# Kernel tuning notes

Measured on AMD Instinct MI355X. Metric: run time of the kernel, lower is better.

The kernel has to match this reference:

```python
import math
import jax, jax.numpy as jnp
import numpy as np

FS = 96000.0
N_BIQUADS = 16
HPF_FREQ_RANGE = (20.0, 500.0)
LPF_FREQ_RANGE = (5000.0, 20000.0)
SHELF_FREQ_RANGE = (50.0, 16000.0)
PEAK_FREQ_RANGE = (100.0, 15000.0)
Q_RANGE = (0.5, 16.0)
GAIN_RANGE = (-24.0, 24.0)
BROADBAND_RANGE = (-60.0, 0.0)


def _denorm_log(norm, lo, hi):
    return jnp.exp(math.log(lo) + norm * (math.log(hi) - math.log(lo)))


def _coef_highpass(fc, Q):
    w0 = 2.0 * math.pi * fc / FS
    alpha = jnp.sin(w0) / (2.0 * Q)
    c = jnp.cos(w0)
    b0 = (1 + c) / 2; b1 = -(1 + c); b2 = (1 + c) / 2
    a0 = 1 + alpha; a1 = -2 * c; a2 = 1 - alpha
    return b0 / a0, b1 / a0, b2 / a0, a1 / a0, a2 / a0


def _coef_lowpass(fc, Q):
    w0 = 2.0 * math.pi * fc / FS
    alpha = jnp.sin(w0) / (2.0 * Q)
    c = jnp.cos(w0)
    b0 = (1 - c) / 2; b1 = 1 - c; b2 = (1 - c) / 2
    a0 = 1 + alpha; a1 = -2 * c; a2 = 1 - alpha
    return b0 / a0, b1 / a0, b2 / a0, a1 / a0, a2 / a0


def _coef_lowshelf(fc, gain_db, Q):
    A = 10.0 ** (gain_db / 40.0)
    w0 = 2.0 * math.pi * fc / FS
    alpha = jnp.sin(w0) / (2.0 * Q)
    c = jnp.cos(w0)
    sA = jnp.sqrt(A)
    b0 = A * (A + 1 - (A - 1) * c + 2 * sA * alpha)
    b1 = 2 * A * (A - 1 - (A + 1) * c)
    b2 = A * (A + 1 - (A - 1) * c - 2 * sA * alpha)
    a0 = A + 1 + (A - 1) * c + 2 * sA * alpha
    a1 = -2 * (A - 1 + (A + 1) * c)
    a2 = A + 1 + (A - 1) * c - 2 * sA * alpha
    return b0 / a0, b1 / a0, b2 / a0, a1 / a0, a2 / a0


def _coef_highshelf(fc, gain_db, Q):
    A = 10.0 ** (gain_db / 40.0)
    w0 = 2.0 * math.pi * fc / FS
    alpha = jnp.sin(w0) / (2.0 * Q)
    c = jnp.cos(w0)
    sA = jnp.sqrt(A)
    b0 = A * (A + 1 + (A - 1) * c + 2 * sA * alpha)
    b1 = -2 * A * (A - 1 + (A + 1) * c)
    b2 = A * (A + 1 + (A - 1) * c - 2 * sA * alpha)
    a0 = A + 1 - (A - 1) * c + 2 * sA * alpha
    a1 = 2 * (A - 1 - (A + 1) * c)
    a2 = A + 1 - (A - 1) * c - 2 * sA * alpha
    return b0 / a0, b1 / a0, b2 / a0, a1 / a0, a2 / a0


def _coef_peak(fc, gain_db, Q):
    A = 10.0 ** (gain_db / 40.0)
    w0 = 2.0 * math.pi * fc / FS
    alpha = jnp.sin(w0) / (2.0 * Q)
    c = jnp.cos(w0)
    b0 = 1 + alpha * A; b1 = -2 * c; b2 = 1 - alpha * A
    a0 = 1 + alpha / A; a1 = -2 * c; a2 = 1 - alpha / A
    return b0 / a0, b1 / a0, b2 / a0, a1 / a0, a2 / a0


def _biquad(x, coefs):
    # x: (B, T); coefs: 5 arrays of shape (B,)
    b0, b1, b2, a1, a2 = coefs

    def step(carry, xt):  # xt: (B,)
        s1, s2 = carry
        y = b0 * xt + s1
        return (b1 * xt - a1 * y + s2, b2 * xt - a2 * y), y

    z = jnp.zeros(x.shape[0], x.dtype)
    _, ys = jax.lax.scan(step, (z, z), x.T)  # ys: (T, B)
    return ys.T


def _chain(audio, params):
    B = audio.shape[0]
    bp = params[:, :N_BIQUADS * 3].reshape(B, N_BIQUADS, 3)
    bb_lo, bb_hi = BROADBAND_RANGE
    in_db = bb_lo + params[:, -2] * (bb_hi - bb_lo)
    out_db = bb_lo + params[:, -1] * (bb_hi - bb_lo)
    x = audio * (10.0 ** (in_db / 20.0))[:, None]

    for i in range(N_BIQUADS):
        fn, gn, qn = bp[:, i, 0], bp[:, i, 1], bp[:, i, 2]
        Q = _denorm_log(qn, *Q_RANGE)
        gain = GAIN_RANGE[0] + gn * (GAIN_RANGE[1] - GAIN_RANGE[0])
        if i == 0:  # HPF
            coefs = _coef_highpass(_denorm_log(fn, *HPF_FREQ_RANGE), Q)
        elif i == 15:  # LPF
            coefs = _coef_lowpass(_denorm_log(fn, *LPF_FREQ_RANGE), Q)
        elif i == 1:  # low shelf
            coefs = _coef_lowshelf(_denorm_log(fn, *SHELF_FREQ_RANGE), gain, Q)
        elif i == 14:  # high shelf
            coefs = _coef_highshelf(_denorm_log(fn, *SHELF_FREQ_RANGE), gain, Q)
        else:  # peaking EQ
            coefs = _coef_peak(_denorm_log(fn, *PEAK_FREQ_RANGE), gain, Q)
        x = _biquad(x, coefs)

    return x * (10.0 ** (out_db / 20.0))[:, None]


def setup_inputs() -> dict:
    key = jax.random.key(0)
    k1, k2 = jax.random.split(key)
    audio = jax.random.normal(k1, (16, 262144), dtype=jnp.float32)
    params = jax.random.uniform(k2, (16, 50), dtype=jnp.float32)
    return {"audio": audio, "params": params}


def reference(audio, params):
    return _chain(audio, params)
```

## Files before the change

### kernel.cpp

```cpp
#include <hip/hip_runtime.h>
#include <math.h>

#define BATCH   16
#define T_LEN   262144
#define NB      16
#define L       64
#define GRP     64
#define SUB     16
#define CHAINS  4
#define NSUB    256
#define NSUP    16
#define NG      64
#define NCHUNK  4096
#define XSTRIDE 68

#define DPI 3.14159265358979323846264338327950288

#define OFF_COEF  0
#define OFF_A64   1536
#define OFF_A1K   17920
#define OFF_A16K  34304
#define OFF_QEND  50688
#define OFF_SARR  181760
#define OFF_P     312832

__device__ inline void stage_coefs(int i, double fn, double gn, double qn,
                                   double& B0, double& B1, double& B2,
                                   double& A1, double& A2) {
    const double FS = 96000.0;
    double Q    = exp(log(0.5) + qn * (log(16.0) - log(0.5)));
    double gain = -24.0 + gn * 48.0;
    double lo, hi;
    if (i == 0)            { lo = 20.0;   hi = 500.0;   }
    else if (i == 15)      { lo = 5000.0; hi = 20000.0; }
    else if (i == 1 || i == 14) { lo = 50.0; hi = 16000.0; }
    else                   { lo = 100.0;  hi = 15000.0; }
    double fc    = exp(log(lo) + fn * (log(hi) - log(lo)));
    double w0    = 2.0 * DPI * fc / FS;
    double alpha = sin(w0) / (2.0 * Q);
    double c     = cos(w0);
    double b0, b1, b2, a0, a1, a2;
    if (i == 0) {
        b0 = (1.0 + c) * 0.5; b1 = -(1.0 + c); b2 = (1.0 + c) * 0.5;
        a0 = 1.0 + alpha; a1 = -2.0 * c; a2 = 1.0 - alpha;
    } else if (i == 15) {
        b0 = (1.0 - c) * 0.5; b1 = 1.0 - c; b2 = (1.0 - c) * 0.5;
        a0 = 1.0 + alpha; a1 = -2.0 * c; a2 = 1.0 - alpha;
    } else if (i == 1) {
        double A = pow(10.0, gain / 40.0), sA = sqrt(A);
        b0 = A * ((A + 1.0) - (A - 1.0) * c + 2.0 * sA * alpha);
        b1 = 2.0 * A * ((A - 1.0) - (A + 1.0) * c);
        b2 = A * ((A + 1.0) - (A - 1.0) * c - 2.0 * sA * alpha);
        a0 = (A + 1.0) + (A - 1.0) * c + 2.0 * sA * alpha;
        a1 = -2.0 * ((A - 1.0) + (A + 1.0) * c);
        a2 = (A + 1.0) + (A - 1.0) * c - 2.0 * sA * alpha;
    } else if (i == 14) {
        double A = pow(10.0, gain / 40.0), sA = sqrt(A);
        b0 = A * ((A + 1.0) + (A - 1.0) * c + 2.0 * sA * alpha);
        b1 = -2.0 * A * ((A - 1.0) + (A + 1.0) * c);
        b2 = A * ((A + 1.0) + (A - 1.0) * c - 2.0 * sA * alpha);
        a0 = (A + 1.0) - (A - 1.0) * c + 2.0 * sA * alpha;
        a1 = 2.0 * ((A - 1.0) - (A + 1.0) * c);
        a2 = (A + 1.0) - (A - 1.0) * c - 2.0 * sA * alpha;
    } else {
        double A = pow(10.0, gain / 40.0);
        b0 = 1.0 + alpha * A; b1 = -2.0 * c; b2 = 1.0 - alpha * A;
        a0 = 1.0 + alpha / A; a1 = -2.0 * c; a2 = 1.0 - alpha / A;
    }
    B0 = b0 / a0; B1 = b1 / a0; B2 = b2 / a0; A1 = a1 / a0; A2 = a2 / a0;
}

__global__ __launch_bounds__(256) void k0_setup(const float* __restrict__ params,
                                                float* __restrict__ coefs,
                                                float* __restrict__ A64,
                                                float* __restrict__ A1K,
                                                float* __restrict__ A16K) {
    int b = blockIdx.x;
    int t = threadIdx.x;
    __shared__ double cf[NB][5];
    __shared__ double M1[32 * 32];
    __shared__ double M2[32 * 32];

    if (t < NB) {
        double B0, B1, B2, A1, A2;
        stage_coefs(t, (double)params[b * 50 + t * 3 + 0],
                       (double)params[b * 50 + t * 3 + 1],
                       (double)params[b * 50 + t * 3 + 2], B0, B1, B2, A1, A2);
        float f0 = (float)B0, f1 = (float)B1, f2 = (float)B2, f3 = (float)A1, f4 = (float)A2;
        cf[t][0] = (double)f0; cf[t][1] = (double)f1; cf[t][2] = (double)f2;
        cf[t][3] = (double)f3; cf[t][4] = (double)f4;
        float* cp = coefs + b * 96 + t * 5;
        cp[0] = f0; cp[1] = f1; cp[2] = f2; cp[3] = f3; cp[4] = f4;
    }
    if (t == NB) {
        double indb = -60.0 + (double)params[b * 50 + 48] * 60.0;
        coefs[b * 96 + 80] = (float)pow(10.0, indb / 20.0);
    }
    if (t == NB + 1) {
        double outdb = -60.0 + (double)params[b * 50 + 49] * 60.0;
        coefs[b * 96 + 81] = (float)pow(10.0, outdb / 20.0);
    }
    __syncthreads();

    if (t < 32) {
        double s1[NB], s2[NB];
#pragma unroll
        for (int i = 0; i < NB; i++) {
            s1[i] = (t == 2 * i) ? 1.0 : 0.0;
            s2[i] = (t == 2 * i + 1) ? 1.0 : 0.0;
        }
        double u = 0.0;
#pragma unroll
        for (int i = 0; i < NB; i++) {
            double y  = cf[i][0] * u + s1[i];
            double n1 = cf[i][1] * u - cf[i][3] * y + s2[i];
            double n2 = cf[i][2] * u - cf[i][4] * y;
            s1[i] = n1; s2[i] = n2; u = y;
        }
#pragma unroll
        for (int i = 0; i < NB; i++) {
            M1[(2 * i) * 32 + t]     = s1[i];
            M1[(2 * i + 1) * 32 + t] = s2[i];
        }
    }
    __syncthreads();

    int c  = t & 31;
    int r0 = t >> 5;
    double* src = M1;
    double* dst = M2;
    for (int sq = 0; sq < 14; sq++) {
        double acc[4] = {0.0, 0.0, 0.0, 0.0};
        for (int k = 0; k < 32; k++) {
            double bv = src[k * 32 + c];
#pragma unroll
            for (int e = 0; e < 4; e++)
                acc[e] += src[(e * 8 + r0) * 32 + k] * bv;
        }
#pragma unroll
        for (int e = 0; e < 4; e++) dst[(e * 8 + r0) * 32 + c] = acc[e];
        __syncthreads();
        { double* tmp = src; src = dst; dst = tmp; }
        float* out_m = (sq == 5) ? A64 : (sq == 9) ? A1K : (sq == 13) ? A16K : nullptr;
        if (out_m) {
#pragma unroll
            for (int e = 0; e < 4; e++) {
                int idx = (e * 8 + r0) * 32 + c;
                out_m[b * 1024 + idx] = (float)src[idx];
            }
        }
        __syncthreads();
    }
}

__device__ __forceinline__ float mv_step_rl(const float* ar, float q, float addv) {
    int qi = __float_as_int(q);
    float qb[32];
#pragma unroll
    for (int t = 0; t < 32; t++)
        qb[t] = __int_as_float(__builtin_amdgcn_readlane(qi, t));
    float acc0 = addv, acc1 = 0.f;
#pragma unroll
    for (int t = 0; t < 32; t += 2) {
        acc0 = fmaf(ar[t], qb[t], acc0);
        acc1 = fmaf(ar[t + 1], qb[t + 1], acc1);
    }
    return acc0 + acc1;
}

__device__ __forceinline__ void load_row32(const float* base, int row, float* ar) {
    const float4* a4 = (const float4*)(base + row * 32);
#pragma unroll
    for (int j = 0; j < 8; j++) {
        float4 v = a4[j];
        ar[4 * j + 0] = v.x; ar[4 * j + 1] = v.y;
        ar[4 * j + 2] = v.z; ar[4 * j + 3] = v.w;
    }
}

__device__ __forceinline__ void stage_audio(const float* __restrict__ gbase,
                                            float* __restrict__ xlds, int lane) {
    const float4* g4 = (const float4*)gbase;
    float4 v[16];
#pragma unroll
    for (int it = 0; it < 16; it++) v[it] = g4[it * 64 + lane];
#pragma unroll
    for (int it = 0; it < 16; it++) {
        int idx = it * 64 + lane;
        int ch = idx >> 4, q = idx & 15;
        *(float4*)&xlds[ch * XSTRIDE + q * 4] = v[it];
    }
}

__global__ __launch_bounds__(64, 1) void k1_pass1(const float* __restrict__ audio,
                                                  const float* __restrict__ coefs,
                                                  const float* __restrict__ A64,
                                                  float* __restrict__ P,
                                                  float* __restrict__ Qend) {
    int blk   = blockIdx.x;
    int batch = blk >> 6;
    int grp   = blk & 63;
    int lane  = threadIdx.x;
    int row   = lane & 31;

    __shared__ float xlds[GRP * XSTRIDE];
    __shared__ float plds[GRP][33];

    stage_audio(audio + (size_t)batch * T_LEN + (size_t)grp * GRP * L, xlds, lane);
    __syncthreads();

    const float* cf = coefs + batch * 96;
    float c0[NB], c1[NB], c2[NB], c3[NB], c4[NB];
#pragma unroll
    for (int i = 0; i < NB; i++) {
        c0[i] = cf[i * 5 + 0]; c1[i] = cf[i * 5 + 1]; c2[i] = cf[i * 5 + 2];
        c3[i] = cf[i * 5 + 3]; c4[i] = cf[i * 5 + 4];
    }
    float ing = cf[80];

    float s1[NB], s2[NB];
#pragma unroll
    for (int i = 0; i < NB; i++) { s1[i] = 0.f; s2[i] = 0.f; }

    float* xrow = &xlds[lane * XSTRIDE];
#pragma unroll 1
    for (int tt = 0; tt < 16; tt++) {
        float4 xv = *(const float4*)&xrow[tt * 4];
        float xs[4] = {xv.x, xv.y, xv.z, xv.w};
#pragma unroll
        for (int j = 0; j < 4; j++) {
            float u = ing * xs[j];
#pragma unroll
            for (int i = 0; i < NB; i++) {
                float y  = fmaf(c0[i], u, s1[i]);
                float n1 = fmaf(c1[i], u, s2[i]); n1 = fmaf(-c3[i], y, n1);
                float n2 = c2[i] * u;             n2 = fmaf(-c4[i], y, n2);
                s1[i] = n1; s2[i] = n2; u = y;
            }
        }
    }

    {
        float* pb = P + ((size_t)(batch * NG + grp)) * 2048;
#pragma unroll
        for (int i = 0; i < NB; i++) {
            pb[(2 * i) * 64 + lane]     = s1[i];
            pb[(2 * i + 1) * 64 + lane] = s2[i];
        }
    }

#pragma unroll
    for (int i = 0; i < NB; i++) {
        plds[lane][2 * i]     = s1[i];
        plds[lane][2 * i + 1] = s2[i];
    }
    __syncthreads();

    float ar[32];
    load_row32(A64 + batch * 1024, row, ar);
    float q0 = 0.f, q1 = 0.f, q2 = 0.f, q3 = 0.f;
#pragma unroll 1
    for (int j = 0; j < SUB; j++) {
        float p0 = plds[0 * SUB + j][row];
        float p1 = plds[1 * SUB + j][row];
        float p2 = plds[2 * SUB + j][row];
        float p3 = plds[3 * SUB + j][row];
        q0 = mv_step_rl(ar, q0, p0);
        q1 = mv_step_rl(ar, q1, p1);
        q2 = mv_step_rl(ar, q2, p2);
        q3 = mv_step_rl(ar, q3, p3);
    }
    if (lane < 32) {
        float* qe = Qend + ((size_t)(batch * NSUB + grp * CHAINS)) * 32 + row;
        qe[0] = q0; qe[32] = q1; qe[64] = q2; qe[96] = q3;
    }
}

__global__ __launch_bounds__(256, 1) void k2_combine(const float* __restrict__ A1K,
                                                     const float* __restrict__ A16K,
                                                     const float* __restrict__ Qend,
                                                     float* __restrict__ Sarr) {
    int batch = blockIdx.x;
    int tid   = threadIdx.x;
    int wave  = tid >> 6;
    int lane  = tid & 63;
    int row   = lane & 31;

    __shared__ float qe[NSUB][32];
    __shared__ float qs[NSUP][32];
    __shared__ float ss[NSUP][32];

    {
        const float4* src4 = (const float4*)(Qend + (size_t)batch * NSUB * 32);
        float4* dst4 = (float4*)&qe[0][0];
        for (int i = tid; i < NSUB * 32 / 4; i += 256) dst4[i] = src4[i];
    }
    float ar1k[32];
    load_row32(A1K + batch * 1024, row, ar1k);
    __syncthreads();

    int s0i = wave * 4;
    {
        float q0 = 0.f, q1 = 0.f, q2 = 0.f, q3 = 0.f;
#pragma unroll 1
        for (int j = 0; j < 16; j++) {
            float p0 = qe[(s0i + 0) * 16 + j][row];
            float p1 = qe[(s0i + 1) * 16 + j][row];
            float p2 = qe[(s0i + 2) * 16 + j][row];
            float p3 = qe[(s0i + 3) * 16 + j][row];
            q0 = mv_step_rl(ar1k, q0, p0);
            q1 = mv_step_rl(ar1k, q1, p1);
            q2 = mv_step_rl(ar1k, q2, p2);
            q3 = mv_step_rl(ar1k, q3, p3);
        }
        if (lane < 32) {
            qs[s0i + 0][row] = q0; qs[s0i + 1][row] = q1;
            qs[s0i + 2][row] = q2; qs[s0i + 3][row] = q3;
        }
    }
    __syncthreads();

    if (wave == 0) {
        float ark[32];
        load_row32(A16K + batch * 1024, row, ark);
        float S = 0.f;
#pragma unroll 1
        for (int s = 0; s < NSUP; s++) {
            if (lane < 32) ss[s][row] = S;
            float addv = qs[s][row];
            S = mv_step_rl(ark, S, addv);
        }
    }
    __syncthreads();

    {
        float q0 = ss[s0i + 0][row];
        float q1 = ss[s0i + 1][row];
        float q2 = ss[s0i + 2][row];
        float q3 = ss[s0i + 3][row];
#pragma unroll 1
        for (int j = 0; j < 16; j++) {
            if (lane < 32) {
                Sarr[((size_t)(batch * NSUB + (s0i + 0) * 16 + j)) * 32 + row] = q0;
                Sarr[((size_t)(batch * NSUB + (s0i + 1) * 16 + j)) * 32 + row] = q1;
                Sarr[((size_t)(batch * NSUB + (s0i + 2) * 16 + j)) * 32 + row] = q2;
                Sarr[((size_t)(batch * NSUB + (s0i + 3) * 16 + j)) * 32 + row] = q3;
            }
            float p0 = qe[(s0i + 0) * 16 + j][row];
            float p1 = qe[(s0i + 1) * 16 + j][row];
            float p2 = qe[(s0i + 2) * 16 + j][row];
            float p3 = qe[(s0i + 3) * 16 + j][row];
            q0 = mv_step_rl(ar1k, q0, p0);
            q1 = mv_step_rl(ar1k, q1, p1);
            q2 = mv_step_rl(ar1k, q2, p2);
            q3 = mv_step_rl(ar1k, q3, p3);
        }
    }
}

__global__ __launch_bounds__(64, 1) void k3_pass2(const float* __restrict__ audio,
                                                  const float* __restrict__ coefs,
                                                  const float* __restrict__ A64,
                                                  const float* __restrict__ P,
                                                  const float* __restrict__ Sarr,
                                                  float* __restrict__ out) {
    int blk   = blockIdx.x;
    int batch = blk >> 6;
    int grp   = blk & 63;
    int lane  = threadIdx.x;
    int row   = lane & 31;

    __shared__ float xlds[GRP * XSTRIDE];
    __shared__ float plds[GRP][33];

    stage_audio(audio + (size_t)batch * T_LEN + (size_t)grp * GRP * L, xlds, lane);

    {
        const float* pb = P + ((size_t)(batch * NG + grp)) * 2048;
        float pv[32];
#pragma unroll
        for (int s = 0; s < 32; s++) pv[s] = pb[s * 64 + lane];
#pragma unroll
        for (int s = 0; s < 32; s++) plds[lane][s] = pv[s];
    }
    __syncthreads();

    {
        float ar[32];
        load_row32(A64 + batch * 1024, row, ar);
        const float* sp = Sarr + ((size_t)(batch * NSUB + grp * CHAINS)) * 32 + row;
        float q0 = sp[0], q1 = sp[32], q2 = sp[64], q3 = sp[96];
#pragma unroll 1
        for (int j = 0; j < SUB; j++) {
            float p0 = plds[0 * SUB + j][row];
            float p1 = plds[1 * SUB + j][row];
            float p2 = plds[2 * SUB + j][row];
            float p3 = plds[3 * SUB + j][row];
            if (lane < 32) {
                plds[0 * SUB + j][row] = q0;
                plds[1 * SUB + j][row] = q1;
                plds[2 * SUB + j][row] = q2;
                plds[3 * SUB + j][row] = q3;
            }
            q0 = mv_step_rl(ar, q0, p0);
            q1 = mv_step_rl(ar, q1, p1);
            q2 = mv_step_rl(ar, q2, p2);
            q3 = mv_step_rl(ar, q3, p3);
        }
    }
    __syncthreads();

    const float* cf = coefs + batch * 96;
    float c0[NB], c1[NB], c2[NB], c3[NB], c4[NB];
#pragma unroll
    for (int i = 0; i < NB; i++) {
        c0[i] = cf[i * 5 + 0]; c1[i] = cf[i * 5 + 1]; c2[i] = cf[i * 5 + 2];
        c3[i] = cf[i * 5 + 3]; c4[i] = cf[i * 5 + 4];
    }
    float ing  = cf[80];
    float outg = cf[81];

    float s1[NB], s2[NB];
#pragma unroll
    for (int i = 0; i < NB; i++) {
        s1[i] = plds[lane][2 * i];
        s2[i] = plds[lane][2 * i + 1];
    }

    float* xrow = &xlds[lane * XSTRIDE];
#pragma unroll 1
    for (int tt = 0; tt < 16; tt++) {
        float4 xv = *(const float4*)&xrow[tt * 4];
        float xs[4] = {xv.x, xv.y, xv.z, xv.w};
        float ys[4];
#pragma unroll
        for (int j = 0; j < 4; j++) {
            float u = ing * xs[j];
#pragma unroll
            for (int i = 0; i < NB; i++) {
                float y  = fmaf(c0[i], u, s1[i]);
                float n1 = fmaf(c1[i], u, s2[i]); n1 = fmaf(-c3[i], y, n1);
                float n2 = c2[i] * u;             n2 = fmaf(-c4[i], y, n2);
                s1[i] = n1; s2[i] = n2; u = y;
            }
            ys[j] = outg * u;
        }
        float4 yv; yv.x = ys[0]; yv.y = ys[1]; yv.z = ys[2]; yv.w = ys[3];
        *(float4*)&xrow[tt * 4] = yv;
    }
    __syncthreads();

    {
        float4* g4 = (float4*)(out + (size_t)batch * T_LEN + (size_t)grp * GRP * L);
#pragma unroll
        for (int it = 0; it < 16; it++) {
            int idx = it * 64 + lane;
            int ch = idx >> 4, q = idx & 15;
            g4[it * 64 + lane] = *(const float4*)&xlds[ch * XSTRIDE + q * 4];
        }
    }
}

extern "C" void kernel_launch(void* const* d_in, const int* in_sizes, int n_in,
                              void* d_out, int out_size, void* d_ws, size_t ws_size,
                              hipStream_t stream) {
    const float* audio  = (const float*)d_in[0];
    const float* params = (const float*)d_in[1];
    float* out = (float*)d_out;
    float* ws  = (float*)d_ws;

    float* coefs = ws + OFF_COEF;
    float* A64   = ws + OFF_A64;
    float* A1K   = ws + OFF_A1K;
    float* A16K  = ws + OFF_A16K;
    float* Qend  = ws + OFF_QEND;
    float* Sarr  = ws + OFF_SARR;
    float* P     = ws + OFF_P;

    k0_setup<<<BATCH, 256, 0, stream>>>(params, coefs, A64, A1K, A16K);
    k1_pass1<<<BATCH * NG, 64, 0, stream>>>(audio, coefs, A64, P, Qend);
    k2_combine<<<BATCH, 256, 0, stream>>>(A1K, A16K, Qend, Sarr);
    k3_pass2<<<BATCH * NG, 64, 0, stream>>>(audio, coefs, A64, P, Sarr, out);
}
```

Measured before the change: 152.1 us.

## Split scan chains across both half-waves and broadcast state via LDS float4 reads

The block-scan hierarchy is regrouped into 8 chains of 8 sub-blocks per group, so both 32-lane halves of each wave process 4 chains each instead of duplicating work. The k2 combine stage uses A^512 and A^8K powers accordingly. The readlane-based broadcast is replaced by writing the state vector to LDS and reading it back as float4, and the first step from a zero state is skipped. This shortens the serial matrix-vector chains and cuts VALU work, at the cost of extra LDS traffic and a larger workspace.

```diff
diff --git a/kernel.cpp b/kernel.cpp
--- a/kernel.cpp
+++ b/kernel.cpp
@@ -6,10 +6,9 @@
 #define NB      16
 #define L       64
 #define GRP     64
-#define SUB     16
-#define CHAINS  4
-#define NSUB    256
-#define NSUP    16
+#define SUB     8
+#define NSUB    512
+#define NSUP    32
 #define NG      64
 #define NCHUNK  4096
 #define XSTRIDE 68
@@ -18,11 +17,11 @@
 
 #define OFF_COEF  0
 #define OFF_A64   1536
-#define OFF_A1K   17920
-#define OFF_A16K  34304
+#define OFF_A512  17920
+#define OFF_A8K   34304
 #define OFF_QEND  50688
-#define OFF_SARR  181760
-#define OFF_P     312832
+#define OFF_SARR  312832
+#define OFF_P     574976
 
 __device__ inline void stage_coefs(int i, double fn, double gn, double qn,
                                    double& B0, double& B1, double& B2,
@@ -73,8 +72,8 @@
 __global__ __launch_bounds__(256) void k0_setup(const float* __restrict__ params,
                                                 float* __restrict__ coefs,
                                                 float* __restrict__ A64,
-                                                float* __restrict__ A1K,
-                                                float* __restrict__ A16K) {
+                                                float* __restrict__ A512,
+                                                float* __restrict__ A8K) {
     int b = blockIdx.x;
     int t = threadIdx.x;
     __shared__ double cf[NB][5];
@@ -129,7 +128,7 @@
     int r0 = t >> 5;
     double* src = M1;
     double* dst = M2;
-    for (int sq = 0; sq < 14; sq++) {
+    for (int sq = 0; sq < 13; sq++) {
         double acc[4] = {0.0, 0.0, 0.0, 0.0};
         for (int k = 0; k < 32; k++) {
             double bv = src[k * 32 + c];
@@ -141,7 +140,7 @@
         for (int e = 0; e < 4; e++) dst[(e * 8 + r0) * 32 + c] = acc[e];
         __syncthreads();
         { double* tmp = src; src = dst; dst = tmp; }
-        float* out_m = (sq == 5) ? A64 : (sq == 9) ? A1K : (sq == 13) ? A16K : nullptr;
+        float* out_m = (sq == 5) ? A64 : (sq == 8) ? A512 : (sq == 12) ? A8K : nullptr;
         if (out_m) {
 #pragma unroll
             for (int e = 0; e < 4; e++) {
@@ -151,6 +150,35 @@
         }
         __syncthreads();
     }
+}
+
+__device__ __forceinline__ void bc_step4(float* qldsw, int row, int cb,
+                                         const float* ar,
+                                         float p0, float p1, float p2, float p3,
+                                         float& q0, float& q1, float& q2, float& q3) {
+    qldsw[(cb + 0) * 32 + row] = q0;
+    qldsw[(cb + 1) * 32 + row] = q1;
+    qldsw[(cb + 2) * 32 + row] = q2;
+    qldsw[(cb + 3) * 32 + row] = q3;
+    const float* qb = qldsw + cb * 32;
+    float a0 = p0, b0 = 0.f, a1 = p1, b1 = 0.f;
+    float a2 = p2, b2 = 0.f, a3 = p3, b3 = 0.f;
+#pragma unroll
+    for (int t4 = 0; t4 < 8; t4++) {
+        float4 v0 = *(const float4*)(qb + 0 * 32 + 4 * t4);
+        float4 v1 = *(const float4*)(qb + 1 * 32 + 4 * t4);
+        float4 v2 = *(const float4*)(qb + 2 * 32 + 4 * t4);
+        float4 v3 = *(const float4*)(qb + 3 * 32 + 4 * t4);
+        a0 = fmaf(ar[4 * t4 + 0], v0.x, a0); b0 = fmaf(ar[4 * t4 + 1], v0.y, b0);
+        a0 = fmaf(ar[4 * t4 + 2], v0.z, a0); b0 = fmaf(ar[4 * t4 + 3], v0.w, b0);
+        a1 = fmaf(ar[4 * t4 + 0], v1.x, a1); b1 = fmaf(ar[4 * t4 + 1], v1.y, b1);
+        a1 = fmaf(ar[4 * t4 + 2], v1.z, a1); b1 = fmaf(ar[4 * t4 + 3], v1.w, b1);
+        a2 = fmaf(ar[4 * t4 + 0], v2.x, a2); b2 = fmaf(ar[4 * t4 + 1], v2.y, b2);
+        a2 = fmaf(ar[4 * t4 + 2], v2.z, a2); b2 = fmaf(ar[4 * t4 + 3], v2.w, b2);
+        a3 = fmaf(ar[4 * t4 + 0], v3.x, a3); b3 = fmaf(ar[4 * t4 + 1], v3.y, b3);
+        a3 = fmaf(ar[4 * t4 + 2], v3.z, a3); b3 = fmaf(ar[4 * t4 + 3], v3.w, b3);
+    }
+    q0 = a0 + b0; q1 = a1 + b1; q2 = a2 + b2; q3 = a3 + b3;
 }
 
 __device__ __forceinline__ float mv_step_rl(const float* ar, float q, float addv) {
@@ -202,9 +230,11 @@
     int grp   = blk & 63;
     int lane  = threadIdx.x;
     int row   = lane & 31;
+    int half  = lane >> 5;
 
     __shared__ float xlds[GRP * XSTRIDE];
     __shared__ float plds[GRP][33];
+    __shared__ float qlds[8 * 32];
 
     stage_audio(audio + (size_t)batch * T_LEN + (size_t)grp * GRP * L, xlds, lane);
     __syncthreads();
@@ -258,26 +288,27 @@
 
     float ar[32];
     load_row32(A64 + batch * 1024, row, ar);
-    float q0 = 0.f, q1 = 0.f, q2 = 0.f, q3 = 0.f;
-#pragma unroll 1
-    for (int j = 0; j < SUB; j++) {
-        float p0 = plds[0 * SUB + j][row];
-        float p1 = plds[1 * SUB + j][row];
-        float p2 = plds[2 * SUB + j][row];
-        float p3 = plds[3 * SUB + j][row];
-        q0 = mv_step_rl(ar, q0, p0);
-        q1 = mv_step_rl(ar, q1, p1);
-        q2 = mv_step_rl(ar, q2, p2);
-        q3 = mv_step_rl(ar, q3, p3);
-    }
-    if (lane < 32) {
-        float* qe = Qend + ((size_t)(batch * NSUB + grp * CHAINS)) * 32 + row;
+    int cb = half * 4;
+    float q0 = plds[(cb + 0) * SUB][row];
+    float q1 = plds[(cb + 1) * SUB][row];
+    float q2 = plds[(cb + 2) * SUB][row];
+    float q3 = plds[(cb + 3) * SUB][row];
+#pragma unroll 1
+    for (int j = 1; j < SUB; j++) {
+        float p0 = plds[(cb + 0) * SUB + j][row];
+        float p1 = plds[(cb + 1) * SUB + j][row];
+        float p2 = plds[(cb + 2) * SUB + j][row];
+        float p3 = plds[(cb + 3) * SUB + j][row];
+        bc_step4(qlds, row, cb, ar, p0, p1, p2, p3, q0, q1, q2, q3);
+    }
+    {
+        float* qe = Qend + ((size_t)(batch * NSUB + grp * 8 + cb)) * 32 + row;
         qe[0] = q0; qe[32] = q1; qe[64] = q2; qe[96] = q3;
     }
 }
 
-__global__ __launch_bounds__(256, 1) void k2_combine(const float* __restrict__ A1K,
-                                                     const float* __restrict__ A16K,
+__global__ __launch_bounds__(256, 1) void k2_combine(const float* __restrict__ A512,
+                                                     const float* __restrict__ A8K,
                                                      const float* __restrict__ Qend,
                                                      float* __restrict__ Sarr) {
     int batch = blockIdx.x;
@@ -285,44 +316,46 @@
     int wave  = tid >> 6;
     int lane  = tid & 63;
     int row   = lane & 31;
+    int half  = lane >> 5;
+    int cb    = half * 4;
 
     __shared__ float qe[NSUB][32];
     __shared__ float qs[NSUP][32];
     __shared__ float ss[NSUP][32];
+    __shared__ float qlds[4][8 * 32];
 
     {
         const float4* src4 = (const float4*)(Qend + (size_t)batch * NSUB * 32);
         float4* dst4 = (float4*)&qe[0][0];
         for (int i = tid; i < NSUB * 32 / 4; i += 256) dst4[i] = src4[i];
     }
-    float ar1k[32];
-    load_row32(A1K + batch * 1024, row, ar1k);
-    __syncthreads();
-
-    int s0i = wave * 4;
-    {
-        float q0 = 0.f, q1 = 0.f, q2 = 0.f, q3 = 0.f;
-#pragma unroll 1
-        for (int j = 0; j < 16; j++) {
-            float p0 = qe[(s0i + 0) * 16 + j][row];
-            float p1 = qe[(s0i + 1) * 16 + j][row];
-            float p2 = qe[(s0i + 2) * 16 + j][row];
-            float p3 = qe[(s0i + 3) * 16 + j][row];
-            q0 = mv_step_rl(ar1k, q0, p0);
-            q1 = mv_step_rl(ar1k, q1, p1);
-            q2 = mv_step_rl(ar1k, q2, p2);
-            q3 = mv_step_rl(ar1k, q3, p3);
-        }
-        if (lane < 32) {
-            qs[s0i + 0][row] = q0; qs[s0i + 1][row] = q1;
-            qs[s0i + 2][row] = q2; qs[s0i + 3][row] = q3;
-        }
+    float ar512[32];
+    load_row32(A512 + batch * 1024, row, ar512);
+    __syncthreads();
+
+    int sbase = wave * 8 + cb;
+
+    {
+        float q0 = qe[(sbase + 0) * 16][row];
+        float q1 = qe[(sbase + 1) * 16][row];
+        float q2 = qe[(sbase + 2) * 16][row];
+        float q3 = qe[(sbase + 3) * 16][row];
+#pragma unroll 1
+        for (int j = 1; j < 16; j++) {
+            float p0 = qe[(sbase + 0) * 16 + j][row];
+            float p1 = qe[(sbase + 1) * 16 + j][row];
+            float p2 = qe[(sbase + 2) * 16 + j][row];
+            float p3 = qe[(sbase + 3) * 16 + j][row];
+            bc_step4(qlds[wave], row, cb, ar512, p0, p1, p2, p3, q0, q1, q2, q3);
+        }
+        qs[sbase + 0][row] = q0; qs[sbase + 1][row] = q1;
+        qs[sbase + 2][row] = q2; qs[sbase + 3][row] = q3;
     }
     __syncthreads();
 
     if (wave == 0) {
         float ark[32];
-        load_row32(A16K + batch * 1024, row, ark);
+        load_row32(A8K + batch * 1024, row, ark);
         float S = 0.f;
 #pragma unroll 1
         for (int s = 0; s < NSUP; s++) {
@@ -334,26 +367,23 @@
     __syncthreads();
 
     {
-        float q0 = ss[s0i + 0][row];
-        float q1 = ss[s0i + 1][row];
-        float q2 = ss[s0i + 2][row];
-        float q3 = ss[s0i + 3][row];
+        float q0 = ss[sbase + 0][row];
+        float q1 = ss[sbase + 1][row];
+        float q2 = ss[sbase + 2][row];
+        float q3 = ss[sbase + 3][row];
 #pragma unroll 1
         for (int j = 0; j < 16; j++) {
-            if (lane < 32) {
-                Sarr[((size_t)(batch * NSUB + (s0i + 0) * 16 + j)) * 32 + row] = q0;
-                Sarr[((size_t)(batch * NSUB + (s0i + 1) * 16 + j)) * 32 + row] = q1;
-                Sarr[((size_t)(batch * NSUB + (s0i + 2) * 16 + j)) * 32 + row] = q2;
-                Sarr[((size_t)(batch * NSUB + (s0i + 3) * 16 + j)) * 32 + row] = q3;
+            Sarr[((size_t)(batch * NSUB + (sbase + 0) * 16 + j)) * 32 + row] = q0;
+            Sarr[((size_t)(batch * NSUB + (sbase + 1) * 16 + j)) * 32 + row] = q1;
+            Sarr[((size_t)(batch * NSUB + (sbase + 2) * 16 + j)) * 32 + row] = q2;
+            Sarr[((size_t)(batch * NSUB + (sbase + 3) * 16 + j)) * 32 + row] = q3;
+            if (j < 15) {
+                float p0 = qe[(sbase + 0) * 16 + j][row];
+                float p1 = qe[(sbase + 1) * 16 + j][row];
+                float p2 = qe[(sbase + 2) * 16 + j][row];
+                float p3 = qe[(sbase + 3) * 16 + j][row];
+                bc_step4(qlds[wave], row, cb, ar512, p0, p1, p2, p3, q0, q1, q2, q3);
             }
-            float p0 = qe[(s0i + 0) * 16 + j][row];
-            float p1 = qe[(s0i + 1) * 16 + j][row];
-            float p2 = qe[(s0i + 2) * 16 + j][row];
-            float p3 = qe[(s0i + 3) * 16 + j][row];
-            q0 = mv_step_rl(ar1k, q0, p0);
-            q1 = mv_step_rl(ar1k, q1, p1);
-            q2 = mv_step_rl(ar1k, q2, p2);
-            q3 = mv_step_rl(ar1k, q3, p3);
         }
     }
 }
@@ -369,9 +399,12 @@
     int grp   = blk & 63;
     int lane  = threadIdx.x;
     int row   = lane & 31;
+    int half  = lane >> 5;
+    int cb    = half * 4;
 
     __shared__ float xlds[GRP * XSTRIDE];
     __shared__ float plds[GRP][33];
+    __shared__ float qlds[8 * 32];
 
     stage_audio(audio + (size_t)batch * T_LEN + (size_t)grp * GRP * L, xlds, lane);
 
@@ -388,24 +421,20 @@
     {
         float ar[32];
         load_row32(A64 + batch * 1024, row, ar);
-        const float* sp = Sarr + ((size_t)(batch * NSUB + grp * CHAINS)) * 32 + row;
+        const float* sp = Sarr + ((size_t)(batch * NSUB + grp * 8 + cb)) * 32 + row;
         float q0 = sp[0], q1 = sp[32], q2 = sp[64], q3 = sp[96];
 #pragma unroll 1
         for (int j = 0; j < SUB; j++) {
-            float p0 = plds[0 * SUB + j][row];
-            float p1 = plds[1 * SUB + j][row];
-            float p2 = plds[2 * SUB + j][row];
-            float p3 = plds[3 * SUB + j][row];
-            if (lane < 32) {
-                plds[0 * SUB + j][row] = q0;
-                plds[1 * SUB + j][row] = q1;
-                plds[2 * SUB + j][row] = q2;
-                plds[3 * SUB + j][row] = q3;
-            }
-            q0 = mv_step_rl(ar, q0, p0);
-            q1 = mv_step_rl(ar, q1, p1);
-            q2 = mv_step_rl(ar, q2, p2);
-            q3 = mv_step_rl(ar, q3, p3);
+            float p0 = plds[(cb + 0) * SUB + j][row];
+            float p1 = plds[(cb + 1) * SUB + j][row];
+            float p2 = plds[(cb + 2) * SUB + j][row];
+            float p3 = plds[(cb + 3) * SUB + j][row];
+            plds[(cb + 0) * SUB + j][row] = q0;
+            plds[(cb + 1) * SUB + j][row] = q1;
+            plds[(cb + 2) * SUB + j][row] = q2;
+            plds[(cb + 3) * SUB + j][row] = q3;
+            if (j < SUB - 1)
+                bc_step4(qlds, row, cb, ar, p0, p1, p2, p3, q0, q1, q2, q3);
         }
     }
     __syncthreads();
@@ -471,14 +500,14 @@
 
     float* coefs = ws + OFF_COEF;
     float* A64   = ws + OFF_A64;
-    float* A1K   = ws + OFF_A1K;
-    float* A16K  = ws + OFF_A16K;
+    float* A512  = ws + OFF_A512;
+    float* A8K   = ws + OFF_A8K;
     float* Qend  = ws + OFF_QEND;
     float* Sarr  = ws + OFF_SARR;
     float* P     = ws + OFF_P;
 
-    k0_setup<<<BATCH, 256, 0, stream>>>(params, coefs, A64, A1K, A16K);
+    k0_setup<<<BATCH, 256, 0, stream>>>(params, coefs, A64, A512, A8K);
     k1_pass1<<<BATCH * NG, 64, 0, stream>>>(audio, coefs, A64, P, Qend);
-    k2_combine<<<BATCH, 256, 0, stream>>>(A1K, A16K, Qend, Sarr);
+    k2_combine<<<BATCH, 256, 0, stream>>>(A512, A8K, Qend, Sarr);
     k3_pass2<<<BATCH * NG, 64, 0, stream>>>(audio, coefs, A64, P, Sarr, out);
 }
```

Result: no change. 152.9 us (+0.6%).
